# Kernel tuning notes

Hardware: AMD Instinct MI355X
Metric: run time of the kernel (lower is better)

The kernel has to match this reference:

```python
import jax, jax.numpy as jnp
import numpy as np

B, T, C = 4, 2048, 512
N_HEADS, HEAD_DIM, TOP_K = 8, 64, 32
SCALE = HEAD_DIM ** -0.5
LN_EPS = 1e-5
# AdaptiveLIFNeuron assumed params (standard adaptive LIF with soft reset)
V_DECAY = 0.9       # membrane decay
TH0 = 1.0           # base threshold
TH_BETA = 0.1       # threshold adaptation strength
ADAPT_DECAY = 0.9   # adaptation variable decay
SG_SLOPE = 4.0      # surrogate-gradient sigmoid slope


def _spike(u):
    # Heaviside forward, sigmoid-surrogate backward (straight-through)
    sg = jax.nn.sigmoid(SG_SLOPE * u)
    hard = (u > 0).astype(u.dtype)
    return jax.lax.stop_gradient(hard - sg) + sg


def setup_inputs() -> dict:
    key = jax.random.key(0)
    ks = jax.random.split(key, 6)
    s = 0.02
    return {
        "x": jax.random.normal(ks[0], (B, T, C), jnp.float32),
        "Wq": jax.random.normal(ks[1], (C, C), jnp.float32) * s,
        "bq": jnp.zeros((C,), jnp.float32),
        "Wk": jax.random.normal(ks[2], (C, C), jnp.float32) * s,
        "bk": jnp.zeros((C,), jnp.float32),
        "Wv": jax.random.normal(ks[3], (C, C), jnp.float32) * s,
        "bv": jnp.zeros((C,), jnp.float32),
        "Wo": jax.random.normal(ks[4], (C, C), jnp.float32) * s,
        "bo": jnp.zeros((C,), jnp.float32),
        "gamma": jnp.ones((C,), jnp.float32),
        "beta": jnp.zeros((C,), jnp.float32),
    }


def reference(x, Wq, bq, Wk, bk, Wv, bv, Wo, bo, gamma, beta):
    Bx, Tx, Cx = x.shape

    def heads(h):  # (B,T,C) -> (B,H,T,hd)
        return h.reshape(Bx, Tx, N_HEADS, HEAD_DIM).transpose(0, 2, 1, 3)

    q = heads(x @ Wq + bq)
    k = heads(x @ Wk + bk)
    v = heads(x @ Wv + bv)

    scores = jnp.einsum("bhqd,bhkd->bhqk", q, k) * SCALE  # (B,H,T,T)
    # top-k masking: softmax over scattered top-k == softmax of full matrix
    # with -inf everywhere except top-k entries (non-selected probs are 0)
    topk_vals, topk_idx = jax.lax.top_k(scores, TOP_K)
    probs_k = jax.nn.softmax(topk_vals, axis=-1)
    attn_probs = jnp.put_along_axis(
        jnp.zeros_like(scores), topk_idx, probs_k, axis=-1, inplace=False
    )

    context = jnp.einsum("bhqk,bhkd->bhqd", attn_probs, v)
    context = context.transpose(0, 2, 1, 3).reshape(Bx, Tx, Cx)

    analog = context @ Wo + bo
    mu = jnp.mean(analog, axis=-1, keepdims=True)
    var = jnp.var(analog, axis=-1, keepdims=True)
    analog = (analog - mu) * jax.lax.rsqrt(var + LN_EPS) * gamma + beta

    # sequential adaptive LIF readout over time
    def step(carry, x_t):  # x_t: (B,C)
        vmem, adapt = carry
        vmem = V_DECAY * vmem + x_t
        th = TH0 + TH_BETA * adapt
        s = _spike(vmem - th)
        vmem = vmem - s * th            # soft reset
        adapt = ADAPT_DECAY * adapt + s
        return (vmem, adapt), s

    init = (jnp.zeros((Bx, Cx), analog.dtype), jnp.zeros((Bx, Cx), analog.dtype))
    _, spikes = jax.lax.scan(step, init, analog.transpose(1, 0, 2))  # (T,B,C)
    out_spikes = spikes.transpose(1, 0, 2)
    return out_spikes, attn_probs
```

## Files before the change

### kernel.cpp

```cpp
#include <hip/hip_runtime.h>
#include <cstdint>
#include <math.h>

#define B_ 4
#define T_ 2048
#define C_ 512
#define H_ 8
#define HD_ 64
#define TOPK_ 32
#define ROWS_ (B_*H_*T_)
#define BT_ (B_*T_)

__global__ __launch_bounds__(256) void qkv_kernel(
    const float* __restrict__ x,
    const float* __restrict__ Wq, const float* __restrict__ bq,
    const float* __restrict__ Wk, const float* __restrict__ bk,
    const float* __restrict__ Wv, const float* __restrict__ bv,
    float* __restrict__ Q, float* __restrict__ K, float* __restrict__ V)
{
    const int which = blockIdx.z;
    const float* W    = (which == 0) ? Wq : (which == 1) ? Wk : Wv;
    const float* bias = (which == 0) ? bq : (which == 1) ? bk : bv;
    float* out        = (which == 0) ? Q  : (which == 1) ? K  : V;

    const int m0 = blockIdx.y * 128;
    const int n0 = blockIdx.x * 128;
    __shared__ float As[16][128];
    __shared__ float Bs[16][128];
    float acc[8][8] = {};
    const int tid = threadIdx.x;
    const int tx = tid & 15, ty = tid >> 4;

    for (int k0 = 0; k0 < C_; k0 += 16) {
        #pragma unroll
        for (int i = 0; i < 2; ++i) {
            int t = tid + i * 256;
            int m  = t >> 2;
            int kq = (t & 3) << 2;
            float4 a4 = *(const float4*)(x + (size_t)(m0 + m) * C_ + k0 + kq);
            As[kq + 0][m] = a4.x; As[kq + 1][m] = a4.y;
            As[kq + 2][m] = a4.z; As[kq + 3][m] = a4.w;
            int kk2 = t >> 5;
            int nq  = (t & 31) << 2;
            *(float4*)&Bs[kk2][nq] = *(const float4*)(W + (size_t)(k0 + kk2) * C_ + n0 + nq);
        }
        __syncthreads();
        #pragma unroll
        for (int k = 0; k < 16; ++k) {
            float a[8], b[8];
            *(float4*)&a[0] = *(const float4*)&As[k][ty * 8];
            *(float4*)&a[4] = *(const float4*)&As[k][ty * 8 + 4];
            *(float4*)&b[0] = *(const float4*)&Bs[k][tx * 8];
            *(float4*)&b[4] = *(const float4*)&Bs[k][tx * 8 + 4];
            #pragma unroll
            for (int i = 0; i < 8; ++i)
                #pragma unroll
                for (int j = 0; j < 8; ++j)
                    acc[i][j] += a[i] * b[j];
        }
        __syncthreads();
    }
    #pragma unroll
    for (int i = 0; i < 8; ++i) {
        int r = m0 + ty * 8 + i;
        int bb = r >> 11, t = r & (T_ - 1);
        #pragma unroll
        for (int j = 0; j < 8; j += 4) {
            int n = n0 + tx * 8 + j;
            int h = n >> 6, d = n & 63;
            float4 v4;
            v4.x = acc[i][j + 0] + bias[n + 0];
            v4.y = acc[i][j + 1] + bias[n + 1];
            v4.z = acc[i][j + 2] + bias[n + 2];
            v4.w = acc[i][j + 3] + bias[n + 3];
            *(float4*)(out + (((size_t)(bb * H_ + h) * T_ + t) << 6) + d) = v4;
        }
    }
}

__global__ __launch_bounds__(256) void scores_kernel(
    const float* __restrict__ Q, const float* __restrict__ K,
    float* __restrict__ S)
{
    const int bh = blockIdx.z;
    const int m0 = blockIdx.y * 128;
    const int n0 = blockIdx.x * 128;
    const float* Qb = Q + ((size_t)bh * T_ << 6);
    const float* Kb = K + ((size_t)bh * T_ << 6);
    __shared__ float Qs[64][128];
    __shared__ float Ks[64][128];
    const int tid = threadIdx.x;
    #pragma unroll
    for (int i = 0; i < 8; ++i) {
        int t = tid + i * 256;
        int m  = t >> 4;
        int dq = (t & 15) << 2;
        float4 q4 = *(const float4*)(Qb + ((size_t)(m0 + m) << 6) + dq);
        Qs[dq + 0][m] = q4.x; Qs[dq + 1][m] = q4.y;
        Qs[dq + 2][m] = q4.z; Qs[dq + 3][m] = q4.w;
        float4 k4 = *(const float4*)(Kb + ((size_t)(n0 + m) << 6) + dq);
        Ks[dq + 0][m] = k4.x; Ks[dq + 1][m] = k4.y;
        Ks[dq + 2][m] = k4.z; Ks[dq + 3][m] = k4.w;
    }
    __syncthreads();
    const int tx = tid & 15, ty = tid >> 4;
    float acc[8][8] = {};
    #pragma unroll 4
    for (int d = 0; d < 64; ++d) {
        float a[8], b[8];
        *(float4*)&a[0] = *(const float4*)&Qs[d][ty * 8];
        *(float4*)&a[4] = *(const float4*)&Qs[d][ty * 8 + 4];
        *(float4*)&b[0] = *(const float4*)&Ks[d][tx * 8];
        *(float4*)&b[4] = *(const float4*)&Ks[d][tx * 8 + 4];
        #pragma unroll
        for (int i = 0; i < 8; ++i)
            #pragma unroll
            for (int j = 0; j < 8; ++j)
                acc[i][j] += a[i] * b[j];
    }
    float* Sb = S + (size_t)bh * T_ * T_;
    #pragma unroll
    for (int i = 0; i < 8; ++i) {
        int m = m0 + ty * 8 + i;
        #pragma unroll
        for (int j = 0; j < 8; j += 4) {
            int n = n0 + tx * 8 + j;
            float4 v4;
            v4.x = acc[i][j + 0] * 0.125f;
            v4.y = acc[i][j + 1] * 0.125f;
            v4.z = acc[i][j + 2] * 0.125f;
            v4.w = acc[i][j + 3] * 0.125f;
            *(float4*)(Sb + (size_t)m * T_ + n) = v4;
        }
    }
}

__device__ __forceinline__ uint32_t f2key(float f) {
    uint32_t u = __float_as_uint(f);
    return (u & 0x80000000u) ? ~u : (u | 0x80000000u);
}
__device__ __forceinline__ float key2f(uint32_t k) {
    uint32_t u = (k & 0x80000000u) ? (k ^ 0x80000000u) : ~k;
    return __uint_as_float(u);
}

__global__ __launch_bounds__(64) void topk_kernel(
    float* __restrict__ S, float* __restrict__ probs_c, int* __restrict__ idx_c)
{
    const size_t row = blockIdx.x;
    float* Srow = S + row * (size_t)T_;
    __shared__ int hist[256];
    __shared__ float selv[32];
    __shared__ int seli[32];
    __shared__ int bc_bin, bc_gt, cnt_gt;
    const int lane = threadIdx.x;

    uint32_t keys[32];
    #pragma unroll
    for (int c = 0; c < 8; ++c) {
        float4 v4 = *(const float4*)(Srow + c * 256 + lane * 4);
        keys[c * 4 + 0] = f2key(v4.x);
        keys[c * 4 + 1] = f2key(v4.y);
        keys[c * 4 + 2] = f2key(v4.z);
        keys[c * 4 + 3] = f2key(v4.w);
    }

    uint32_t prefix = 0;
    int kk = TOPK_;
    #pragma unroll
    for (int pass = 0; pass < 4; ++pass) {
        const int shift = 24 - pass * 8;
        hist[lane] = 0; hist[lane + 64] = 0; hist[lane + 128] = 0; hist[lane + 192] = 0;
        __syncthreads();
        #pragma unroll
        for (int e = 0; e < 32; ++e) {
            uint32_t key = keys[e];
            bool cand = (pass == 0) || (((key ^ prefix) >> (shift + 8)) == 0);
            if (cand) atomicAdd(&hist[(key >> shift) & 255], 1);
        }
        __syncthreads();
        int h0 = hist[lane * 4 + 0], h1 = hist[lane * 4 + 1];
        int h2 = hist[lane * 4 + 2], h3 = hist[lane * 4 + 3];
        int lsum = h0 + h1 + h2 + h3;
        int suf = lsum;
        #pragma unroll
        for (int off = 1; off < 64; off <<= 1) {
            int v = __shfl_down(suf, off);
            if (lane + off < 64) suf += v;
        }
        int a3 = suf - lsum;
        int a2 = a3 + h3;
        int a1 = a2 + h2;
        int a0 = a1 + h1;
        if (a3 < kk && kk <= a3 + h3) { bc_bin = lane * 4 + 3; bc_gt = a3; }
        if (a2 < kk && kk <= a2 + h2) { bc_bin = lane * 4 + 2; bc_gt = a2; }
        if (a1 < kk && kk <= a1 + h1) { bc_bin = lane * 4 + 1; bc_gt = a1; }
        if (a0 < kk && kk <= a0 + h0) { bc_bin = lane * 4 + 0; bc_gt = a0; }
        __syncthreads();
        prefix |= ((uint32_t)bc_bin) << shift;
        kk -= bc_gt;
        __syncthreads();
    }

    if (lane == 0) cnt_gt = 0;
    __syncthreads();
    int eq_local = 0;
    #pragma unroll
    for (int e = 0; e < 32; ++e) {
        uint32_t key = keys[e];
        if (key > prefix) {
            int p = atomicAdd(&cnt_gt, 1);
            if (p < 32) {
                selv[p] = key2f(key);
                seli[p] = (e >> 2) * 256 + lane * 4 + (e & 3);
            }
        } else if (key == prefix) {
            eq_local++;
        }
    }
    __syncthreads();
    const int G = cnt_gt;
    int sc = eq_local;
    #pragma unroll
    for (int off = 1; off < 64; off <<= 1) {
        int v = __shfl_up(sc, off);
        if (lane >= off) sc += v;
    }
    int r = sc - eq_local;
    #pragma unroll
    for (int e = 0; e < 32; ++e) {
        if (keys[e] == prefix) {
            if (r < kk && (G + r) < 32) {
                selv[G + r] = key2f(prefix);
                seli[G + r] = (e >> 2) * 256 + lane * 4 + (e & 3);
            }
            ++r;
        }
    }
    __syncthreads();

    float v = (lane < 32) ? selv[lane] : -3.0e38f;
    float mx = v;
    #pragma unroll
    for (int off = 16; off >= 1; off >>= 1)
        mx = fmaxf(mx, __shfl_xor(mx, off, 32));
    float ex = (lane < 32) ? expf(v - mx) : 0.0f;
    float sm = ex;
    #pragma unroll
    for (int off = 16; off >= 1; off >>= 1)
        sm += __shfl_xor(sm, off, 32);
    float p = ex / sm;
    if (lane < 32) {
        probs_c[row * 32 + lane] = p;
        idx_c[row * 32 + lane] = seli[lane];
        selv[lane] = p;
    }
    __syncthreads();

    float4 z4 = {0.f, 0.f, 0.f, 0.f};
    #pragma unroll
    for (int c = 0; c < 8; ++c)
        *(float4*)(Srow + c * 256 + lane * 4) = z4;
    __syncthreads();
    if (lane < 32) Srow[seli[lane]] = selv[lane];
}

__global__ __launch_bounds__(256) void context_kernel(
    const float* __restrict__ V, const float* __restrict__ probs_c,
    const int* __restrict__ idx_c, float* __restrict__ ctx)
{
    const int wid = blockIdx.x * 4 + (threadIdx.x >> 6);
    const int lane = threadIdx.x & 63;
    const int bh = wid >> 11, t = wid & (T_ - 1);
    const float* Vb = V + ((size_t)bh * T_ << 6);
    const float* pr = probs_c + (size_t)wid * 32;
    const int* ir = idx_c + (size_t)wid * 32;
    float acc = 0.f;
    #pragma unroll 8
    for (int j = 0; j < 32; ++j) {
        float p = pr[j];
        int ix = ir[j];
        acc += p * Vb[((size_t)ix << 6) + lane];
    }
    const int b = bh >> 3, h = bh & 7;
    ctx[(size_t)(b * T_ + t) * C_ + h * 64 + lane] = acc;
}

__global__ __launch_bounds__(256) void wo_kernel(
    const float* __restrict__ A, const float* __restrict__ W,
    const float* __restrict__ bias, float* __restrict__ out)
{
    const int m0 = blockIdx.y * 128;
    const int n0 = blockIdx.x * 128;
    __shared__ float As[16][128];
    __shared__ float Bs[16][128];
    float acc[8][8] = {};
    const int tid = threadIdx.x;
    const int tx = tid & 15, ty = tid >> 4;

    for (int k0 = 0; k0 < C_; k0 += 16) {
        #pragma unroll
        for (int i = 0; i < 2; ++i) {
            int t = tid + i * 256;
            int m  = t >> 2;
            int kq = (t & 3) << 2;
            float4 a4 = *(const float4*)(A + (size_t)(m0 + m) * C_ + k0 + kq);
            As[kq + 0][m] = a4.x; As[kq + 1][m] = a4.y;
            As[kq + 2][m] = a4.z; As[kq + 3][m] = a4.w;
            int kk2 = t >> 5;
            int nq  = (t & 31) << 2;
            *(float4*)&Bs[kk2][nq] = *(const float4*)(W + (size_t)(k0 + kk2) * C_ + n0 + nq);
        }
        __syncthreads();
        #pragma unroll
        for (int k = 0; k < 16; ++k) {
            float a[8], b[8];
            *(float4*)&a[0] = *(const float4*)&As[k][ty * 8];
            *(float4*)&a[4] = *(const float4*)&As[k][ty * 8 + 4];
            *(float4*)&b[0] = *(const float4*)&Bs[k][tx * 8];
            *(float4*)&b[4] = *(const float4*)&Bs[k][tx * 8 + 4];
            #pragma unroll
            for (int i = 0; i < 8; ++i)
                #pragma unroll
                for (int j = 0; j < 8; ++j)
                    acc[i][j] += a[i] * b[j];
        }
        __syncthreads();
    }
    #pragma unroll
    for (int i = 0; i < 8; ++i) {
        int r = m0 + ty * 8 + i;
        #pragma unroll
        for (int j = 0; j < 8; j += 4) {
            int n = n0 + tx * 8 + j;
            float4 v4;
            v4.x = acc[i][j + 0] + bias[n + 0];
            v4.y = acc[i][j + 1] + bias[n + 1];
            v4.z = acc[i][j + 2] + bias[n + 2];
            v4.w = acc[i][j + 3] + bias[n + 3];
            *(float4*)(out + (size_t)r * C_ + n) = v4;
        }
    }
}

__global__ __launch_bounds__(256) void ln_kernel(
    float* __restrict__ a, const float* __restrict__ gamma, const float* __restrict__ beta)
{
    const int row = blockIdx.x * 4 + (threadIdx.x >> 6);
    const int lane = threadIdx.x & 63;
    float* ar = a + (size_t)row * C_;
    float x[8];
    *(float4*)&x[0] = *(const float4*)(ar + lane * 8);
    *(float4*)&x[4] = *(const float4*)(ar + lane * 8 + 4);
    float s = 0.f;
    #pragma unroll
    for (int i = 0; i < 8; ++i) s += x[i];
    #pragma unroll
    for (int off = 32; off >= 1; off >>= 1) s += __shfl_xor(s, off);
    float mu = s * (1.0f / C_);
    float vs = 0.f;
    #pragma unroll
    for (int i = 0; i < 8; ++i) { float d = x[i] - mu; vs += d * d; }
    #pragma unroll
    for (int off = 32; off >= 1; off >>= 1) vs += __shfl_xor(vs, off);
    float rs = rsqrtf(vs * (1.0f / C_) + 1e-5f);
    float g[8], bt[8];
    *(float4*)&g[0]  = *(const float4*)(gamma + lane * 8);
    *(float4*)&g[4]  = *(const float4*)(gamma + lane * 8 + 4);
    *(float4*)&bt[0] = *(const float4*)(beta + lane * 8);
    *(float4*)&bt[4] = *(const float4*)(beta + lane * 8 + 4);
    #pragma unroll
    for (int i = 0; i < 8; ++i) x[i] = (x[i] - mu) * rs * g[i] + bt[i];
    *(float4*)(ar + lane * 8)     = *(float4*)&x[0];
    *(float4*)(ar + lane * 8 + 4) = *(float4*)&x[4];
}

#define LIF_BATCH 32
__global__ __launch_bounds__(64) void lif_kernel(float* __restrict__ a)
{
    const int wid = blockIdx.x;
    const int b = wid >> 3;
    const int c = ((wid & 7) << 6) | threadIdx.x;
    float* base = a + (size_t)b * T_ * C_ + c;

    float xb[2][LIF_BATCH];
    #pragma unroll
    for (int j = 0; j < LIF_BATCH; ++j)
        xb[0][j] = base[(size_t)j * C_];

    float vmem = 0.f, adapt = 0.f;
    #pragma unroll 1
    for (int t0 = 0; t0 < T_; t0 += LIF_BATCH) {
        const int cur = (t0 / LIF_BATCH) & 1;
        if (t0 + LIF_BATCH < T_) {
            #pragma unroll
            for (int j = 0; j < LIF_BATCH; ++j)
                xb[cur ^ 1][j] = base[(size_t)(t0 + LIF_BATCH + j) * C_];
        }
        #pragma unroll
        for (int j = 0; j < LIF_BATCH; ++j) {
            float x = xb[cur][j];
            vmem = fmaf(0.9f, vmem, x);
            float th = fmaf(0.1f, adapt, 1.0f);
            float s = (vmem - th) > 0.f ? 1.f : 0.f;
            vmem -= s * th;
            adapt = fmaf(0.9f, adapt, s);
            xb[cur][j] = s;
        }
        #pragma unroll
        for (int j = 0; j < LIF_BATCH; ++j)
            base[(size_t)(t0 + j) * C_] = xb[cur][j];
    }
}

extern "C" void kernel_launch(void* const* d_in, const int* in_sizes, int n_in,
                              void* d_out, int out_size, void* d_ws, size_t ws_size,
                              hipStream_t stream)
{
    const float* x     = (const float*)d_in[0];
    const float* Wq    = (const float*)d_in[1];
    const float* bq    = (const float*)d_in[2];
    const float* Wk    = (const float*)d_in[3];
    const float* bk    = (const float*)d_in[4];
    const float* Wv    = (const float*)d_in[5];
    const float* bv    = (const float*)d_in[6];
    const float* Wo    = (const float*)d_in[7];
    const float* bo    = (const float*)d_in[8];
    const float* gamma = (const float*)d_in[9];
    const float* beta  = (const float*)d_in[10];

    float* out    = (float*)d_out;
    float* spikes = out;
    float* probs  = out + (size_t)B_ * T_ * C_;

    float* ws = (float*)d_ws;
    const size_t NQ = (size_t)B_ * H_ * T_ * HD_;
    float* Qb      = ws;
    float* Kb      = ws + NQ;
    float* Vb      = ws + 2 * NQ;
    float* ctx     = ws + 3 * NQ;
    float* probs_c = ws + 4 * NQ;
    int*   idx_c   = (int*)(ws + 4 * NQ + (size_t)ROWS_ * 32);

    qkv_kernel<<<dim3(4, 64, 3), 256, 0, stream>>>(x, Wq, bq, Wk, bk, Wv, bv, Qb, Kb, Vb);
    scores_kernel<<<dim3(16, 16, 32), 256, 0, stream>>>(Qb, Kb, probs);
    topk_kernel<<<dim3(ROWS_), 64, 0, stream>>>(probs, probs_c, idx_c);
    context_kernel<<<dim3(ROWS_ / 4), 256, 0, stream>>>(Vb, probs_c, idx_c, ctx);
    wo_kernel<<<dim3(4, 64), 256, 0, stream>>>(ctx, Wo, bo, spikes);
    ln_kernel<<<dim3(BT_ / 4), 256, 0, stream>>>(spikes, gamma, beta);
    lif_kernel<<<dim3(32), 64, 0, stream>>>(spikes);
}
```

Measured before the change: 1.421 ms.

## Fuse QK scores with register-resident top-k radix select, store K transposed

Result: slower. 1.673 ms (+17.7%).

```diff
diff --git a/kernel.cpp b/kernel.cpp
--- a/kernel.cpp
+++ b/kernel.cpp
@@ -16,12 +16,11 @@
     const float* __restrict__ Wq, const float* __restrict__ bq,
     const float* __restrict__ Wk, const float* __restrict__ bk,
     const float* __restrict__ Wv, const float* __restrict__ bv,
-    float* __restrict__ Q, float* __restrict__ K, float* __restrict__ V)
+    float* __restrict__ Q, float* __restrict__ Kt, float* __restrict__ V)
 {
     const int which = blockIdx.z;
     const float* W    = (which == 0) ? Wq : (which == 1) ? Wk : Wv;
     const float* bias = (which == 0) ? bq : (which == 1) ? bk : bv;
-    float* out        = (which == 0) ? Q  : (which == 1) ? K  : V;
 
     const int m0 = blockIdx.y * 128;
     const int n0 = blockIdx.x * 128;
@@ -60,209 +59,250 @@
         }
         __syncthreads();
     }
-    #pragma unroll
-    for (int i = 0; i < 8; ++i) {
-        int r = m0 + ty * 8 + i;
-        int bb = r >> 11, t = r & (T_ - 1);
-        #pragma unroll
-        for (int j = 0; j < 8; j += 4) {
-            int n = n0 + tx * 8 + j;
+
+    const int bb = m0 >> 11;
+    const int t0 = (m0 & (T_ - 1)) + ty * 8;
+
+    if (which == 1) {
+        #pragma unroll
+        for (int jj = 0; jj < 8; ++jj) {
+            int n = n0 + tx * 8 + jj;
             int h = n >> 6, d = n & 63;
-            float4 v4;
-            v4.x = acc[i][j + 0] + bias[n + 0];
-            v4.y = acc[i][j + 1] + bias[n + 1];
-            v4.z = acc[i][j + 2] + bias[n + 2];
-            v4.w = acc[i][j + 3] + bias[n + 3];
-            *(float4*)(out + (((size_t)(bb * H_ + h) * T_ + t) << 6) + d) = v4;
-        }
-    }
-}
-
-__global__ __launch_bounds__(256) void scores_kernel(
-    const float* __restrict__ Q, const float* __restrict__ K,
-    float* __restrict__ S)
-{
-    const int bh = blockIdx.z;
-    const int m0 = blockIdx.y * 128;
-    const int n0 = blockIdx.x * 128;
-    const float* Qb = Q + ((size_t)bh * T_ << 6);
-    const float* Kb = K + ((size_t)bh * T_ << 6);
-    __shared__ float Qs[64][128];
-    __shared__ float Ks[64][128];
-    const int tid = threadIdx.x;
-    #pragma unroll
-    for (int i = 0; i < 8; ++i) {
-        int t = tid + i * 256;
-        int m  = t >> 4;
-        int dq = (t & 15) << 2;
-        float4 q4 = *(const float4*)(Qb + ((size_t)(m0 + m) << 6) + dq);
-        Qs[dq + 0][m] = q4.x; Qs[dq + 1][m] = q4.y;
-        Qs[dq + 2][m] = q4.z; Qs[dq + 3][m] = q4.w;
-        float4 k4 = *(const float4*)(Kb + ((size_t)(n0 + m) << 6) + dq);
-        Ks[dq + 0][m] = k4.x; Ks[dq + 1][m] = k4.y;
-        Ks[dq + 2][m] = k4.z; Ks[dq + 3][m] = k4.w;
-    }
-    __syncthreads();
-    const int tx = tid & 15, ty = tid >> 4;
-    float acc[8][8] = {};
-    #pragma unroll 4
+            float bv_ = bias[n];
+            float* dst = Kt + (((size_t)(bb * H_ + h) * HD_ + d) << 11) + t0;
+            float4 lo, hi;
+            lo.x = acc[0][jj] + bv_; lo.y = acc[1][jj] + bv_;
+            lo.z = acc[2][jj] + bv_; lo.w = acc[3][jj] + bv_;
+            hi.x = acc[4][jj] + bv_; hi.y = acc[5][jj] + bv_;
+            hi.z = acc[6][jj] + bv_; hi.w = acc[7][jj] + bv_;
+            *(float4*)(dst)     = lo;
+            *(float4*)(dst + 4) = hi;
+        }
+    } else {
+        float* out = (which == 0) ? Q : V;
+        #pragma unroll
+        for (int i = 0; i < 8; ++i) {
+            int t = t0 + i;
+            #pragma unroll
+            for (int j = 0; j < 8; j += 4) {
+                int n = n0 + tx * 8 + j;
+                int h = n >> 6, d = n & 63;
+                float4 v4;
+                v4.x = acc[i][j + 0] + bias[n + 0];
+                v4.y = acc[i][j + 1] + bias[n + 1];
+                v4.z = acc[i][j + 2] + bias[n + 2];
+                v4.w = acc[i][j + 3] + bias[n + 3];
+                *(float4*)(out + (((size_t)(bb * H_ + h) * T_ + t) << 6) + d) = v4;
+            }
+        }
+    }
+}
+
+__device__ __forceinline__ unsigned int f2key(float f) {
+    unsigned int u = __float_as_uint(f);
+    return (u & 0x80000000u) ? ~u : (u | 0x80000000u);
+}
+__device__ __forceinline__ float key2f(unsigned int k) {
+    unsigned int u = (k & 0x80000000u) ? (k ^ 0x80000000u) : ~k;
+    return __uint_as_float(u);
+}
+
+__global__ __launch_bounds__(256, 2) void fused_attn_topk(
+    const float* __restrict__ Q, const float* __restrict__ Kt,
+    float* __restrict__ S, float* __restrict__ probs_c, int* __restrict__ idx_c)
+{
+    const int tid  = threadIdx.x;
+    const int wave = tid >> 6, lane = tid & 63;
+    const int m0 = blockIdx.x * 16;
+    const int bh = blockIdx.y;
+
+    __shared__ float Qs[64][20];
+    __shared__ int hist[16][256];
+    __shared__ unsigned int pref_s[16];
+    __shared__ int kk_s[16];
+    __shared__ int gcnt[16], eqc[16];
+    __shared__ float selv[16][32];
+    __shared__ int   seli[16][32];
+    __shared__ float selv2[16][32];
+    __shared__ int   seli2[16][32];
+    __shared__ int   eqcol[16][64];
+
+    {
+        int tok = tid >> 4;
+        int dq  = (tid & 15) << 2;
+        float4 q4 = *(const float4*)(Q + (((size_t)bh * T_ + m0 + tok) << 6) + dq);
+        Qs[dq + 0][tok] = q4.x; Qs[dq + 1][tok] = q4.y;
+        Qs[dq + 2][tok] = q4.z; Qs[dq + 3][tok] = q4.w;
+    }
+    if (tid < 16) { pref_s[tid] = 0u; kk_s[tid] = TOPK_; gcnt[tid] = 0; eqc[tid] = 0; }
+    __syncthreads();
+
+    float acc[16][8];
+    #pragma unroll
+    for (int r = 0; r < 16; ++r)
+        #pragma unroll
+        for (int e = 0; e < 8; ++e) acc[r][e] = 0.f;
+
+    const float* ktp = Kt + ((size_t)bh * HD_ << 11) + wave * 512 + lane * 4;
+    #pragma unroll 2
     for (int d = 0; d < 64; ++d) {
-        float a[8], b[8];
-        *(float4*)&a[0] = *(const float4*)&Qs[d][ty * 8];
-        *(float4*)&a[4] = *(const float4*)&Qs[d][ty * 8 + 4];
-        *(float4*)&b[0] = *(const float4*)&Ks[d][tx * 8];
-        *(float4*)&b[4] = *(const float4*)&Ks[d][tx * 8 + 4];
-        #pragma unroll
-        for (int i = 0; i < 8; ++i)
-            #pragma unroll
-            for (int j = 0; j < 8; ++j)
-                acc[i][j] += a[i] * b[j];
-    }
-    float* Sb = S + (size_t)bh * T_ * T_;
-    #pragma unroll
-    for (int i = 0; i < 8; ++i) {
-        int m = m0 + ty * 8 + i;
-        #pragma unroll
-        for (int j = 0; j < 8; j += 4) {
-            int n = n0 + tx * 8 + j;
-            float4 v4;
-            v4.x = acc[i][j + 0] * 0.125f;
-            v4.y = acc[i][j + 1] * 0.125f;
-            v4.z = acc[i][j + 2] * 0.125f;
-            v4.w = acc[i][j + 3] * 0.125f;
-            *(float4*)(Sb + (size_t)m * T_ + n) = v4;
-        }
-    }
-}
-
-__device__ __forceinline__ uint32_t f2key(float f) {
-    uint32_t u = __float_as_uint(f);
-    return (u & 0x80000000u) ? ~u : (u | 0x80000000u);
-}
-__device__ __forceinline__ float key2f(uint32_t k) {
-    uint32_t u = (k & 0x80000000u) ? (k ^ 0x80000000u) : ~k;
-    return __uint_as_float(u);
-}
-
-__global__ __launch_bounds__(64) void topk_kernel(
-    float* __restrict__ S, float* __restrict__ probs_c, int* __restrict__ idx_c)
-{
-    const size_t row = blockIdx.x;
-    float* Srow = S + row * (size_t)T_;
-    __shared__ int hist[256];
-    __shared__ float selv[32];
-    __shared__ int seli[32];
-    __shared__ int bc_bin, bc_gt, cnt_gt;
-    const int lane = threadIdx.x;
-
-    uint32_t keys[32];
-    #pragma unroll
-    for (int c = 0; c < 8; ++c) {
-        float4 v4 = *(const float4*)(Srow + c * 256 + lane * 4);
-        keys[c * 4 + 0] = f2key(v4.x);
-        keys[c * 4 + 1] = f2key(v4.y);
-        keys[c * 4 + 2] = f2key(v4.z);
-        keys[c * 4 + 3] = f2key(v4.w);
-    }
-
-    uint32_t prefix = 0;
-    int kk = TOPK_;
-    #pragma unroll
+        float4 k0 = *(const float4*)(ktp);
+        float4 k1 = *(const float4*)(ktp + 256);
+        ktp += 2048;
+        float qv[16];
+        *(float4*)&qv[0]  = *(const float4*)&Qs[d][0];
+        *(float4*)&qv[4]  = *(const float4*)&Qs[d][4];
+        *(float4*)&qv[8]  = *(const float4*)&Qs[d][8];
+        *(float4*)&qv[12] = *(const float4*)&Qs[d][12];
+        #pragma unroll
+        for (int r = 0; r < 16; ++r) {
+            acc[r][0] = fmaf(qv[r], k0.x, acc[r][0]);
+            acc[r][1] = fmaf(qv[r], k0.y, acc[r][1]);
+            acc[r][2] = fmaf(qv[r], k0.z, acc[r][2]);
+            acc[r][3] = fmaf(qv[r], k0.w, acc[r][3]);
+            acc[r][4] = fmaf(qv[r], k1.x, acc[r][4]);
+            acc[r][5] = fmaf(qv[r], k1.y, acc[r][5]);
+            acc[r][6] = fmaf(qv[r], k1.z, acc[r][6]);
+            acc[r][7] = fmaf(qv[r], k1.w, acc[r][7]);
+        }
+    }
+    #pragma unroll
+    for (int r = 0; r < 16; ++r)
+        #pragma unroll
+        for (int e = 0; e < 8; ++e) acc[r][e] *= 0.125f;
+
     for (int pass = 0; pass < 4; ++pass) {
         const int shift = 24 - pass * 8;
-        hist[lane] = 0; hist[lane + 64] = 0; hist[lane + 128] = 0; hist[lane + 192] = 0;
-        __syncthreads();
-        #pragma unroll
-        for (int e = 0; e < 32; ++e) {
-            uint32_t key = keys[e];
-            bool cand = (pass == 0) || (((key ^ prefix) >> (shift + 8)) == 0);
-            if (cand) atomicAdd(&hist[(key >> shift) & 255], 1);
-        }
-        __syncthreads();
-        int h0 = hist[lane * 4 + 0], h1 = hist[lane * 4 + 1];
-        int h2 = hist[lane * 4 + 2], h3 = hist[lane * 4 + 3];
-        int lsum = h0 + h1 + h2 + h3;
-        int suf = lsum;
-        #pragma unroll
-        for (int off = 1; off < 64; off <<= 1) {
-            int v = __shfl_down(suf, off);
-            if (lane + off < 64) suf += v;
-        }
-        int a3 = suf - lsum;
-        int a2 = a3 + h3;
-        int a1 = a2 + h2;
-        int a0 = a1 + h1;
-        if (a3 < kk && kk <= a3 + h3) { bc_bin = lane * 4 + 3; bc_gt = a3; }
-        if (a2 < kk && kk <= a2 + h2) { bc_bin = lane * 4 + 2; bc_gt = a2; }
-        if (a1 < kk && kk <= a1 + h1) { bc_bin = lane * 4 + 1; bc_gt = a1; }
-        if (a0 < kk && kk <= a0 + h0) { bc_bin = lane * 4 + 0; bc_gt = a0; }
-        __syncthreads();
-        prefix |= ((uint32_t)bc_bin) << shift;
-        kk -= bc_gt;
-        __syncthreads();
-    }
-
-    if (lane == 0) cnt_gt = 0;
-    __syncthreads();
-    int eq_local = 0;
-    #pragma unroll
-    for (int e = 0; e < 32; ++e) {
-        uint32_t key = keys[e];
-        if (key > prefix) {
-            int p = atomicAdd(&cnt_gt, 1);
-            if (p < 32) {
-                selv[p] = key2f(key);
-                seli[p] = (e >> 2) * 256 + lane * 4 + (e & 3);
+        unsigned int pr[16];
+        #pragma unroll
+        for (int r = 0; r < 16; ++r) pr[r] = pref_s[r];
+        #pragma unroll
+        for (int i = 0; i < 16; ++i) ((int*)hist)[tid + i * 256] = 0;
+        __syncthreads();
+        #pragma unroll
+        for (int r = 0; r < 16; ++r) {
+            #pragma unroll
+            for (int e = 0; e < 8; ++e) {
+                unsigned int k = f2key(acc[r][e]);
+                bool cand = (pass == 0) || (((k ^ pr[r]) >> (shift + 8)) == 0);
+                if (cand) atomicAdd(&hist[r][(k >> shift) & 255], 1);
             }
-        } else if (key == prefix) {
-            eq_local++;
-        }
-    }
-    __syncthreads();
-    const int G = cnt_gt;
-    int sc = eq_local;
-    #pragma unroll
-    for (int off = 1; off < 64; off <<= 1) {
-        int v = __shfl_up(sc, off);
-        if (lane >= off) sc += v;
-    }
-    int r = sc - eq_local;
-    #pragma unroll
-    for (int e = 0; e < 32; ++e) {
-        if (keys[e] == prefix) {
-            if (r < kk && (G + r) < 32) {
-                selv[G + r] = key2f(prefix);
-                seli[G + r] = (e >> 2) * 256 + lane * 4 + (e & 3);
+        }
+        __syncthreads();
+        #pragma unroll
+        for (int rr = 0; rr < 4; ++rr) {
+            const int row = wave * 4 + rr;
+            const int kcur = kk_s[row];
+            int h0 = hist[row][lane * 4 + 0], h1 = hist[row][lane * 4 + 1];
+            int h2 = hist[row][lane * 4 + 2], h3 = hist[row][lane * 4 + 3];
+            int lsum = h0 + h1 + h2 + h3;
+            int suf = lsum;
+            #pragma unroll
+            for (int off = 1; off < 64; off <<= 1) {
+                int v = __shfl_down(suf, off);
+                if (lane + off < 64) suf += v;
             }
-            ++r;
-        }
-    }
-    __syncthreads();
-
-    float v = (lane < 32) ? selv[lane] : -3.0e38f;
-    float mx = v;
-    #pragma unroll
-    for (int off = 16; off >= 1; off >>= 1)
-        mx = fmaxf(mx, __shfl_xor(mx, off, 32));
-    float ex = (lane < 32) ? expf(v - mx) : 0.0f;
-    float sm = ex;
-    #pragma unroll
-    for (int off = 16; off >= 1; off >>= 1)
-        sm += __shfl_xor(sm, off, 32);
-    float p = ex / sm;
-    if (lane < 32) {
-        probs_c[row * 32 + lane] = p;
-        idx_c[row * 32 + lane] = seli[lane];
-        selv[lane] = p;
-    }
-    __syncthreads();
-
+            int a3 = suf - lsum;
+            int a2 = a3 + h3;
+            int a1 = a2 + h2;
+            int a0 = a1 + h1;
+            if (a3 < kcur && kcur <= a3 + h3) { pref_s[row] |= (unsigned)(lane*4+3) << shift; kk_s[row] = kcur - a3; }
+            if (a2 < kcur && kcur <= a2 + h2) { pref_s[row] |= (unsigned)(lane*4+2) << shift; kk_s[row] = kcur - a2; }
+            if (a1 < kcur && kcur <= a1 + h1) { pref_s[row] |= (unsigned)(lane*4+1) << shift; kk_s[row] = kcur - a1; }
+            if (a0 < kcur && kcur <= a0 + h0) { pref_s[row] |= (unsigned)(lane*4+0) << shift; kk_s[row] = kcur - a0; }
+        }
+        __syncthreads();
+    }
+
+    unsigned int thr[16];
+    #pragma unroll
+    for (int r = 0; r < 16; ++r) thr[r] = pref_s[r];
+    const int colb = wave * 512 + lane * 4;
+    #pragma unroll
+    for (int r = 0; r < 16; ++r) {
+        #pragma unroll
+        for (int e = 0; e < 8; ++e) {
+            unsigned int k = f2key(acc[r][e]);
+            int col = colb + ((e >> 2) << 8) + (e & 3);
+            if (k > thr[r]) {
+                int p = atomicAdd(&gcnt[r], 1);
+                selv[r][p] = key2f(k);
+                seli[r][p] = col;
+            } else if (k == thr[r]) {
+                int ee = atomicAdd(&eqc[r], 1);
+                if (ee < 64) eqcol[r][ee] = col;
+            }
+        }
+    }
+    __syncthreads();
+    if (tid < 16) {
+        int row = tid, g = gcnt[row], need = TOPK_ - g;
+        int cnt = eqc[row]; if (cnt > 64) cnt = 64;
+        float tv = key2f(pref_s[row]);
+        int last = -1;
+        for (int it = 0; it < need; ++it) {
+            int mn = 0x7fffffff;
+            for (int e = 0; e < cnt; ++e) {
+                int c = eqcol[row][e];
+                if (c > last && c < mn) mn = c;
+            }
+            selv[row][g + it] = tv;
+            seli[row][g + it] = mn;
+            last = mn;
+        }
+    }
+    __syncthreads();
+
+    #pragma unroll
+    for (int base = 0; base < 512; base += 256) {
+        int idx = base + tid;
+        int row = idx >> 5, slot = idx & 31;
+        float v = selv[row][slot];
+        int   c = seli[row][slot];
+        unsigned int k = f2key(v);
+        int rank = 0;
+        #pragma unroll
+        for (int s = 0; s < 32; ++s) {
+            unsigned int ko = f2key(selv[row][s]);
+            int co = seli[row][s];
+            rank += (ko > k) || (ko == k && co < c);
+        }
+        selv2[row][rank] = v;
+        seli2[row][rank] = c;
+    }
+    __syncthreads();
+
+    #pragma unroll
+    for (int base = 0; base < 512; base += 256) {
+        int idx = base + tid;
+        int row = idx >> 5, slot = idx & 31;
+        float v = selv2[row][slot];
+        float mx = v;
+        #pragma unroll
+        for (int off = 16; off >= 1; off >>= 1) mx = fmaxf(mx, __shfl_xor(mx, off, 32));
+        float ex = expf(v - mx);
+        float sm = ex;
+        #pragma unroll
+        for (int off = 16; off >= 1; off >>= 1) sm += __shfl_xor(sm, off, 32);
+        float p = ex / sm;
+        selv2[row][slot] = p;
+        size_t grow = (size_t)(bh * T_ + m0 + row) * 32 + slot;
+        probs_c[grow] = p;
+        idx_c[grow]   = seli2[row][slot];
+    }
+    __syncthreads();
+
+    float* Sb = S + (size_t)bh * T_ * T_ + (size_t)m0 * T_;
     float4 z4 = {0.f, 0.f, 0.f, 0.f};
     #pragma unroll
-    for (int c = 0; c < 8; ++c)
-        *(float4*)(Srow + c * 256 + lane * 4) = z4;
-    __syncthreads();
-    if (lane < 32) Srow[seli[lane]] = selv[lane];
+    for (int i = 0; i < 32; ++i) ((float4*)Sb)[tid + i * 256] = z4;
+    __syncthreads();
+    #pragma unroll
+    for (int base = 0; base < 512; base += 256) {
+        int idx = base + tid;
+        int row = idx >> 5, slot = idx & 31;
+        Sb[(size_t)row * T_ + seli2[row][slot]] = selv2[row][slot];
+    }
 }
 
 __global__ __launch_bounds__(256) void context_kernel(
@@ -433,19 +473,20 @@
     float* spikes = out;
     float* probs  = out + (size_t)B_ * T_ * C_;
 
-    float* ws = (float*)d_ws;
     const size_t NQ = (size_t)B_ * H_ * T_ * HD_;
-    float* Qb      = ws;
-    float* Kb      = ws + NQ;
-    float* Vb      = ws + 2 * NQ;
-    float* ctx     = ws + 3 * NQ;
-    float* probs_c = ws + 4 * NQ;
-    int*   idx_c   = (int*)(ws + 4 * NQ + (size_t)ROWS_ * 32);
-
-    qkv_kernel<<<dim3(4, 64, 3), 256, 0, stream>>>(x, Wq, bq, Wk, bk, Wv, bv, Qb, Kb, Vb);
-    scores_kernel<<<dim3(16, 16, 32), 256, 0, stream>>>(Qb, Kb, probs);
-    topk_kernel<<<dim3(ROWS_), 64, 0, stream>>>(probs, probs_c, idx_c);
-    context_kernel<<<dim3(ROWS_ / 4), 256, 0, stream>>>(Vb, probs_c, idx_c, ctx);
+    char* w = (char*)d_ws;
+    float* Vf      = (float*)w;  w += NQ * 4;
+    float* ctx     = (float*)w;  w += (size_t)BT_ * C_ * 4;
+    float* probs_c = (float*)w;  w += (size_t)ROWS_ * 32 * 4;
+    int*   idx_c   = (int*)w;    w += (size_t)ROWS_ * 32 * 4;
+    float* Qf      = (float*)w;  w += NQ * 4;
+    float* Ktf     = (float*)w;  w += NQ * 4;
+
+    qkv_kernel<<<dim3(4, 64, 3), 256, 0, stream>>>(x, Wq, bq, Wk, bk, Wv, bv,
+                                                   Qf, Ktf, Vf);
+    fused_attn_topk<<<dim3(T_ / 16, B_ * H_), 256, 0, stream>>>(Qf, Ktf,
+                                                                probs, probs_c, idx_c);
+    context_kernel<<<dim3(ROWS_ / 4), 256, 0, stream>>>(Vf, probs_c, idx_c, ctx);
     wo_kernel<<<dim3(4, 64), 256, 0, stream>>>(ctx, Wo, bo, spikes);
     ln_kernel<<<dim3(BT_ / 4), 256, 0, stream>>>(spikes, gamma, beta);
     lif_kernel<<<dim3(32), 64, 0, stream>>>(spikes);
```
